# Kernel optimization log

Measured on AMD Instinct MI355X. Metric: run time of the kernel, lower is better.

Reference implementation:

```python
import jax, jax.numpy as jnp
import numpy as np

NUM_UNITS = 256
DIM_HIDDEN = 1024
NUM_GROUPS = 8
BATCH = 768
MASK_P = 0.2


def setup_inputs() -> dict:
    key = jax.random.key(0)
    k_x, k_m, k_w1, k_w2 = jax.random.split(key, 4)
    x = jax.random.normal(k_x, (BATCH, NUM_UNITS), dtype=jnp.float32)
    mask = jax.random.bernoulli(k_m, MASK_P, (BATCH, NUM_UNITS))  # True = drop unit
    # Xavier-normal initialized linear layers (zeros bias), as in _weights_init.
    s1 = float(np.sqrt(2.0 / (NUM_UNITS + DIM_HIDDEN)))
    s2 = float(np.sqrt(2.0 / (DIM_HIDDEN + NUM_UNITS)))
    W1 = jax.random.normal(k_w1, (NUM_UNITS, DIM_HIDDEN), dtype=jnp.float32) * s1
    b1 = jnp.zeros((DIM_HIDDEN,), dtype=jnp.float32)
    W2 = jax.random.normal(k_w2, (DIM_HIDDEN, NUM_UNITS), dtype=jnp.float32) * s2
    b2 = jnp.zeros((NUM_UNITS,), dtype=jnp.float32)
    temperature = jnp.ones((NUM_UNITS,), dtype=jnp.float32)
    return {"x": x, "mask": mask, "W1": W1, "b1": b1, "W2": W2, "b2": b2,
            "temperature": temperature}


def _mlp(v, W1, b1, W2, b2):
    h = jax.nn.leaky_relu(v @ W1 + b1, negative_slope=0.01)
    return h @ W2 + b2


def reference(x, mask, W1, b1, W2, b2, temperature):
    B = x.shape[0]
    key_ = _mlp(x, W1, b1, W2, b2)                      # [B, U]
    x_masked = jnp.where(mask, 0.0, x)                  # UnitMask: drop units
    query = _mlp(x_masked, W1, b1, W2, b2)              # [B, U]
    # w[i, j, u] = -|key[j,u] - query[i,u]| * temperature[u]
    w = -jnp.abs(key_[None, :, :] - query[:, None, :]) * temperature
    eye = jnp.eye(B, dtype=bool)[:, :, None]
    w = jnp.where(eye, -jnp.inf, w)
    w = w.reshape(B, B // NUM_GROUPS, NUM_GROUPS, NUM_UNITS)
    w = jax.nn.softmax(w, axis=1)
    w = w.reshape(B, B, NUM_UNITS) / 8
    return (w, mask)
```

## Files before the change

kernel.cpp:

```cpp
#include <hip/hip_runtime.h>
#include <hip/hip_bf16.h>
#include <math.h>

#define NU   256
#define DH   1024
#define NG   8
#define BB   768
#define J1N  (BB/NG)
#define UC   16

__global__ __launch_bounds__(256) void build_x2(const float* __restrict__ x,
                                                const int* __restrict__ mask,
                                                float* __restrict__ X2) {
    int idx = blockIdx.x * 256 + threadIdx.x;
    int r = idx >> 8;
    int c = idx & 255;
    if (r < BB) {
        X2[idx] = x[idx];
    } else {
        int src = (r - BB) * NU + c;
        X2[idx] = mask[src] ? 0.0f : x[src];
    }
}

__global__ __launch_bounds__(256) void gemm_bias(const float* __restrict__ A,
                                                 const float* __restrict__ B,
                                                 const float* __restrict__ bias,
                                                 float* __restrict__ C,
                                                 int M, int N, int K, int leaky) {
    const int BK = 16;
    __shared__ float As[BK][64 + 1];
    __shared__ float Bs[BK][64];
    int t  = threadIdx.x;
    int tx = t & 15;
    int ty = t >> 4;
    int m0 = blockIdx.y * 64;
    int n0 = blockIdx.x * 64;

    float acc[4][4] = {};

    for (int k0 = 0; k0 < K; k0 += BK) {
        {
            int r = t >> 2;
            int c = (t & 3) * 4;
            const float4 a = *(const float4*)&A[(size_t)(m0 + r) * K + k0 + c];
            As[c + 0][r] = a.x;
            As[c + 1][r] = a.y;
            As[c + 2][r] = a.z;
            As[c + 3][r] = a.w;
        }
        {
            int r = t >> 4;
            int c = (t & 15) * 4;
            *(float4*)&Bs[r][c] = *(const float4*)&B[(size_t)(k0 + r) * N + n0 + c];
        }
        __syncthreads();
        #pragma unroll
        for (int k = 0; k < BK; ++k) {
            float a[4], b[4];
            #pragma unroll
            for (int q = 0; q < 4; ++q) a[q] = As[k][ty * 4 + q];
            #pragma unroll
            for (int q = 0; q < 4; ++q) b[q] = Bs[k][tx * 4 + q];
            #pragma unroll
            for (int im = 0; im < 4; ++im)
                #pragma unroll
                for (int in = 0; in < 4; ++in)
                    acc[im][in] = fmaf(a[im], b[in], acc[im][in]);
        }
        __syncthreads();
    }

    #pragma unroll
    for (int im = 0; im < 4; ++im) {
        int m = m0 + ty * 4 + im;
        #pragma unroll
        for (int in = 0; in < 4; ++in) {
            int n = n0 + tx * 4 + in;
            float v = acc[im][in] + bias[n];
            if (leaky) v = v > 0.0f ? v : 0.01f * v;
            C[(size_t)m * N + n] = v;
        }
    }
}

__global__ __launch_bounds__(256) void attn_kernel(const float* __restrict__ KQ,
                                                   const float* __restrict__ temp,
                                                   float* __restrict__ out) {
    __shared__ float s[BB * UC];
    __shared__ float s_q[UC];
    __shared__ float s_t[UC];

    const int uc = blockIdx.x;
    const int i  = blockIdx.y;
    const int t  = threadIdx.x;

    const float* key   = KQ;
    const float* query = KQ + (size_t)BB * NU;

    if (t < UC) {
        s_q[t] = query[(size_t)i * NU + uc * UC + t];
        s_t[t] = temp[uc * UC + t];
    }
    __syncthreads();

    for (int idx = t; idx < BB * UC; idx += 256) {
        int j = idx >> 4;
        int u = idx & (UC - 1);
        float kv = key[(size_t)j * NU + uc * UC + u];
        float lg = -fabsf(kv - s_q[u]) * s_t[u];
        if (j == i) lg = -1e30f;
        s[idx] = lg;
    }
    __syncthreads();

    if (t < NG * UC) {
        int j2 = t >> 4;
        int u  = t & (UC - 1);
        int base = j2 * UC + u;
        const int stride = NG * UC;
        float m = -1e30f;
        #pragma unroll 4
        for (int j1 = 0; j1 < J1N; ++j1)
            m = fmaxf(m, s[base + j1 * stride]);
        float sum = 0.0f;
        #pragma unroll 4
        for (int j1 = 0; j1 < J1N; ++j1) {
            float e = __expf(s[base + j1 * stride] - m);
            s[base + j1 * stride] = e;
            sum += e;
        }
        float inv = 0.125f / sum;
        #pragma unroll 4
        for (int j1 = 0; j1 < J1N; ++j1)
            s[base + j1 * stride] *= inv;
    }
    __syncthreads();

    float* o = out + (size_t)i * BB * NU + uc * UC;
    for (int idx = t; idx < BB * UC; idx += 256) {
        int j = idx >> 4;
        int u = idx & (UC - 1);
        o[(size_t)j * NU + u] = s[idx];
    }
}

__global__ __launch_bounds__(256) void mask_out(const int* __restrict__ mask,
                                                float* __restrict__ out) {
    int idx = blockIdx.x * 256 + threadIdx.x;
    out[idx] = mask[idx] ? 1.0f : 0.0f;
}

extern "C" void kernel_launch(void* const* d_in, const int* in_sizes, int n_in,
                              void* d_out, int out_size, void* d_ws, size_t ws_size,
                              hipStream_t stream) {
    const float* x    = (const float*)d_in[0];
    const int*   mask = (const int*)d_in[1];
    const float* W1   = (const float*)d_in[2];
    const float* b1   = (const float*)d_in[3];
    const float* W2   = (const float*)d_in[4];
    const float* b2   = (const float*)d_in[5];
    const float* temp = (const float*)d_in[6];
    float* out = (float*)d_out;

    float* ws = (float*)d_ws;
    float* X2 = ws;
    float* H  = X2 + 2 * BB * NU;
    float* KQ = H + 2 * BB * DH;

    build_x2<<<dim3(2 * BB * NU / 256), dim3(256), 0, stream>>>(x, mask, X2);

    gemm_bias<<<dim3(DH / 64, 2 * BB / 64), dim3(256), 0, stream>>>(
        X2, W1, b1, H, 2 * BB, DH, NU, 1);

    gemm_bias<<<dim3(NU / 64, 2 * BB / 64), dim3(256), 0, stream>>>(
        H, W2, b2, KQ, 2 * BB, NU, DH, 0);

    attn_kernel<<<dim3(NU / UC, BB), dim3(256), 0, stream>>>(KQ, temp, out);

    mask_out<<<dim3(BB * NU / 256), dim3(256), 0, stream>>>(
        mask, out + (size_t)BB * BB * NU);
}
```

Baseline: 832.0 us.

## Split softmax into per-row stats pass and recompute-and-write pass with coalesced stores

Replaces the shared-memory softmax kernel with two kernels. The first computes per-group exp sums for each query row; the second recomputes the exponentials and writes normalized weights with full-row float4 nontemporal stores. The old kernel wrote 16-float strided chunks per block, so the aim is a fully coalesced, streaming write of the large output. The cost is computing the exponentials twice and launching an extra kernel. The max subtraction is dropped, which relies on logits being non-positive.

```diff
diff --git a/kernel.cpp b/kernel.cpp
--- a/kernel.cpp
+++ b/kernel.cpp
@@ -1,13 +1,14 @@
 #include <hip/hip_runtime.h>
-#include <hip/hip_bf16.h>
 #include <math.h>
 
 #define NU   256
 #define DH   1024
 #define NG   8
 #define BB   768
-#define J1N  (BB/NG)
-#define UC   16
+#define NU4  64
+#define JCH  96
+
+typedef float nfloat4 __attribute__((ext_vector_type(4)));
 
 __global__ __launch_bounds__(256) void build_x2(const float* __restrict__ x,
                                                 const int* __restrict__ mask,
@@ -84,64 +85,87 @@
     }
 }
 
-__global__ __launch_bounds__(256) void attn_kernel(const float* __restrict__ KQ,
-                                                   const float* __restrict__ temp,
-                                                   float* __restrict__ out) {
-    __shared__ float s[BB * UC];
-    __shared__ float s_q[UC];
-    __shared__ float s_t[UC];
-
-    const int uc = blockIdx.x;
+__global__ __launch_bounds__(256) void stats_kernel(const float* __restrict__ KQ,
+                                                    const float* __restrict__ temp,
+                                                    float* __restrict__ scale) {
+    const int i  = blockIdx.x;
+    const int t  = threadIdx.x;
+    const int u4 = t & 63;
+    const int r  = t >> 6;
+
+    const float4* key4 = (const float4*)KQ;
+    const float4* qry4 = (const float4*)(KQ + (size_t)BB * NU);
+    const float4 q  = qry4[(size_t)i * NU4 + u4];
+    const float4 tp = ((const float4*)temp)[u4];
+
+    float4 sa = make_float4(0.f, 0.f, 0.f, 0.f);
+    float4 sb = make_float4(0.f, 0.f, 0.f, 0.f);
+
+    #pragma unroll 4
+    for (int k = 0; k < 192; k += 2) {
+        const int jA = r + 4 * k;
+        const int jB = jA + 4;
+        const float4 ka = key4[(size_t)jA * NU4 + u4];
+        const float4 kb = key4[(size_t)jB * NU4 + u4];
+        if (jA != i) {
+            sa.x += __expf(-fabsf(ka.x - q.x) * tp.x);
+            sa.y += __expf(-fabsf(ka.y - q.y) * tp.y);
+            sa.z += __expf(-fabsf(ka.z - q.z) * tp.z);
+            sa.w += __expf(-fabsf(ka.w - q.w) * tp.w);
+        }
+        if (jB != i) {
+            sb.x += __expf(-fabsf(kb.x - q.x) * tp.x);
+            sb.y += __expf(-fabsf(kb.y - q.y) * tp.y);
+            sb.z += __expf(-fabsf(kb.z - q.z) * tp.z);
+            sb.w += __expf(-fabsf(kb.w - q.w) * tp.w);
+        }
+    }
+
+    float4 ia = make_float4(0.125f / sa.x, 0.125f / sa.y, 0.125f / sa.z, 0.125f / sa.w);
+    float4 ib = make_float4(0.125f / sb.x, 0.125f / sb.y, 0.125f / sb.z, 0.125f / sb.w);
+    ((float4*)scale)[((size_t)i * NG + r) * NU4 + u4]     = ia;
+    ((float4*)scale)[((size_t)i * NG + r + 4) * NU4 + u4] = ib;
+}
+
+__global__ __launch_bounds__(256) void attn_write(const float* __restrict__ KQ,
+                                                  const float* __restrict__ temp,
+                                                  const float* __restrict__ scale,
+                                                  float* __restrict__ out) {
+    const int jc = blockIdx.x;
     const int i  = blockIdx.y;
     const int t  = threadIdx.x;
-
-    const float* key   = KQ;
-    const float* query = KQ + (size_t)BB * NU;
-
-    if (t < UC) {
-        s_q[t] = query[(size_t)i * NU + uc * UC + t];
-        s_t[t] = temp[uc * UC + t];
-    }
-    __syncthreads();
-
-    for (int idx = t; idx < BB * UC; idx += 256) {
-        int j = idx >> 4;
-        int u = idx & (UC - 1);
-        float kv = key[(size_t)j * NU + uc * UC + u];
-        float lg = -fabsf(kv - s_q[u]) * s_t[u];
-        if (j == i) lg = -1e30f;
-        s[idx] = lg;
-    }
-    __syncthreads();
-
-    if (t < NG * UC) {
-        int j2 = t >> 4;
-        int u  = t & (UC - 1);
-        int base = j2 * UC + u;
-        const int stride = NG * UC;
-        float m = -1e30f;
-        #pragma unroll 4
-        for (int j1 = 0; j1 < J1N; ++j1)
-            m = fmaxf(m, s[base + j1 * stride]);
-        float sum = 0.0f;
-        #pragma unroll 4
-        for (int j1 = 0; j1 < J1N; ++j1) {
-            float e = __expf(s[base + j1 * stride] - m);
-            s[base + j1 * stride] = e;
-            sum += e;
-        }
-        float inv = 0.125f / sum;
-        #pragma unroll 4
-        for (int j1 = 0; j1 < J1N; ++j1)
-            s[base + j1 * stride] *= inv;
-    }
-    __syncthreads();
-
-    float* o = out + (size_t)i * BB * NU + uc * UC;
-    for (int idx = t; idx < BB * UC; idx += 256) {
-        int j = idx >> 4;
-        int u = idx & (UC - 1);
-        o[(size_t)j * NU + u] = s[idx];
+    const int u4 = t & 63;
+    const int r  = t >> 6;
+    const int j0 = jc * JCH;
+
+    const float4* key4 = (const float4*)KQ;
+    const float4* qry4 = (const float4*)(KQ + (size_t)BB * NU);
+    const float4 q  = qry4[(size_t)i * NU4 + u4];
+    const float4 tp = ((const float4*)temp)[u4];
+    const float4 va = ((const float4*)scale)[((size_t)i * NG + r) * NU4 + u4];
+    const float4 vb = ((const float4*)scale)[((size_t)i * NG + r + 4) * NU4 + u4];
+
+    nfloat4* o4 = (nfloat4*)out + (size_t)i * BB * NU4;
+
+    #pragma unroll 4
+    for (int k = 0; k < 24; k += 2) {
+        const int jA = j0 + r + 4 * k;
+        const int jB = jA + 4;
+        const float4 ka = key4[(size_t)jA * NU4 + u4];
+        const float4 kb = key4[(size_t)jB * NU4 + u4];
+        nfloat4 ea, eb;
+        ea.x = __expf(-fabsf(ka.x - q.x) * tp.x) * va.x;
+        ea.y = __expf(-fabsf(ka.y - q.y) * tp.y) * va.y;
+        ea.z = __expf(-fabsf(ka.z - q.z) * tp.z) * va.z;
+        ea.w = __expf(-fabsf(ka.w - q.w) * tp.w) * va.w;
+        eb.x = __expf(-fabsf(kb.x - q.x) * tp.x) * vb.x;
+        eb.y = __expf(-fabsf(kb.y - q.y) * tp.y) * vb.y;
+        eb.z = __expf(-fabsf(kb.z - q.z) * tp.z) * vb.z;
+        eb.w = __expf(-fabsf(kb.w - q.w) * tp.w) * vb.w;
+        if (jA == i) ea = (nfloat4)0.0f;
+        if (jB == i) eb = (nfloat4)0.0f;
+        __builtin_nontemporal_store(ea, &o4[(size_t)jA * NU4 + u4]);
+        __builtin_nontemporal_store(eb, &o4[(size_t)jB * NU4 + u4]);
     }
 }
 
@@ -167,6 +191,7 @@
     float* X2 = ws;
     float* H  = X2 + 2 * BB * NU;
     float* KQ = H + 2 * BB * DH;
+    float* scale = H;
 
     build_x2<<<dim3(2 * BB * NU / 256), dim3(256), 0, stream>>>(x, mask, X2);
 
@@ -176,7 +201,9 @@
     gemm_bias<<<dim3(NU / 64, 2 * BB / 64), dim3(256), 0, stream>>>(
         H, W2, b2, KQ, 2 * BB, NU, DH, 0);
 
-    attn_kernel<<<dim3(NU / UC, BB), dim3(256), 0, stream>>>(KQ, temp, out);
+    stats_kernel<<<dim3(BB), dim3(256), 0, stream>>>(KQ, temp, scale);
+
+    attn_write<<<dim3(BB / JCH, BB), dim3(256), 0, stream>>>(KQ, temp, scale, out);
 
     mask_out<<<dim3(BB * NU / 256), dim3(256), 0, stream>>>(
         mask, out + (size_t)BB * BB * NU);
```

Result: faster. 736.5 us (-11.5%).
